# Kernel tuning notes

Hardware: AMD Instinct MI355X
Metric: run time of the kernel (lower is better)

The kernel has to match this reference:

```python
import jax, jax.numpy as jnp
import numpy as np

B, T, C, H = 8, 1024, 768, 12
HD = C // H
EPS = 1e-5
NEG = jnp.finfo(jnp.float32).min


def layer_norm(x, scale, bias):
    mu = jnp.mean(x, axis=-1, keepdims=True)
    var = jnp.mean(jnp.square(x - mu), axis=-1, keepdims=True)
    return (x - mu) * jax.lax.rsqrt(var + EPS) * scale + bias


def setup_inputs() -> dict:
    key = jax.random.key(0)
    ks = jax.random.split(key, 8)
    s = lambda fan_in: 1.0 / np.sqrt(fan_in)
    x = jax.random.normal(ks[0], (B, T, C), dtype=jnp.float32)
    mask = jnp.tril(jnp.ones((T, T), dtype=bool))[None, None, :, :]
    return {
        "x": x,
        "mask": mask,
        "ln1_scale": jnp.ones((C,), jnp.float32),
        "ln1_bias": jnp.zeros((C,), jnp.float32),
        "w_qkv": jax.random.normal(ks[1], (C, 3 * C), jnp.float32) * s(C),
        "b_qkv": jnp.zeros((3 * C,), jnp.float32),
        "w_attn_proj": jax.random.normal(ks[2], (C, C), jnp.float32) * s(C),
        "b_attn_proj": jnp.zeros((C,), jnp.float32),
        "ln2_scale": jnp.ones((C,), jnp.float32),
        "ln2_bias": jnp.zeros((C,), jnp.float32),
        "w_fc": jax.random.normal(ks[3], (C, 4 * C), jnp.float32) * s(C),
        "b_fc": jnp.zeros((4 * C,), jnp.float32),
        "w_mlp_proj": jax.random.normal(ks[4], (4 * C, C), jnp.float32) * s(4 * C),
        "b_mlp_proj": jnp.zeros((C,), jnp.float32),
    }


def reference(x, mask, ln1_scale, ln1_bias, w_qkv, b_qkv, w_attn_proj,
              b_attn_proj, ln2_scale, ln2_bias, w_fc, b_fc, w_mlp_proj,
              b_mlp_proj):
    # --- attention branch (pre-LN) ---
    h = layer_norm(x, ln1_scale, ln1_bias)
    qkv = jnp.einsum('btc,cd->btd', h, w_qkv) + b_qkv      # [B,T,3C]
    qkv = qkv.reshape(B, T, 3 * H, HD)
    q, k, v = jnp.array_split(qkv, 3, axis=2)              # each [B,T,H,HD]
    scale = 1.0 / jnp.sqrt(jnp.float32(HD))
    attn = jnp.einsum('bqhd,bkhd->bhqk', q, k) * scale     # [B,H,T,T]
    attn = jnp.where(mask, attn, NEG)
    attn = jax.nn.softmax(attn, axis=-1)
    ctx = jnp.einsum('bhqk,bkhd->bqhd', attn, v).reshape(B, T, C)
    attn_out = jnp.einsum('btc,cd->btd', ctx, w_attn_proj) + b_attn_proj
    x = x + attn_out
    # --- MLP branch (pre-LN) ---
    h = layer_norm(x, ln2_scale, ln2_bias)
    h = jax.nn.gelu(jnp.einsum('btc,cf->btf', h, w_fc) + b_fc)  # tanh approx, as flax default
    mlp_out = jnp.einsum('btf,fc->btc', h, w_mlp_proj) + b_mlp_proj
    return x + mlp_out
```

## Files before the change

kernel.cpp:

```cpp
#include <hip/hip_runtime.h>
#include <hip/hip_bf16.h>
#include <cstdint>
#include <math.h>

#define BB 8
#define TT 1024
#define CC 768
#define HH 12
#define MROWS (BB*TT)

typedef __hip_bfloat16 bf16;
typedef __attribute__((ext_vector_type(8))) __bf16 bf16x8;
typedef __attribute__((ext_vector_type(4))) float f32x4;

#define MFMA16(a,b,c) __builtin_amdgcn_mfma_f32_16x16x32_bf16(a,b,c,0,0,0)

__device__ __forceinline__ void lds_barrier() {
  asm volatile("s_waitcnt lgkmcnt(0)\n\ts_barrier" ::: "memory");
}

__global__ __launch_bounds__(256) void ln_kernel(
    const float* __restrict__ x, const float* __restrict__ scale,
    const float* __restrict__ bias, bf16* __restrict__ out)
{
  int row = blockIdx.x;
  const float* xr = x + (size_t)row * CC;
  float v[3];
  float s = 0.f, s2 = 0.f;
  for (int i = 0; i < 3; i++) {
    v[i] = xr[threadIdx.x + i*256];
    s += v[i]; s2 += v[i]*v[i];
  }
  for (int m = 1; m < 64; m <<= 1) { s += __shfl_xor(s, m); s2 += __shfl_xor(s2, m); }
  __shared__ float ssum[4], ssum2[4];
  int w = threadIdx.x >> 6;
  if ((threadIdx.x & 63) == 0) { ssum[w] = s; ssum2[w] = s2; }
  __syncthreads();
  s = ssum[0]+ssum[1]+ssum[2]+ssum[3];
  s2 = ssum2[0]+ssum2[1]+ssum2[2]+ssum2[3];
  float mu = s * (1.f/CC);
  float var = s2 * (1.f/CC) - mu*mu;
  float rs = rsqrtf(var + 1e-5f);
  bf16* orow = out + (size_t)row * CC;
  for (int i = 0; i < 3; i++) {
    int c = threadIdx.x + i*256;
    orow[c] = __float2bfloat16((v[i]-mu)*rs*scale[c] + bias[c]);
  }
}

__global__ __launch_bounds__(256) void wtrans_all(
    const float* __restrict__ s0, const float* __restrict__ s1,
    const float* __restrict__ s2, const float* __restrict__ s3,
    bf16* __restrict__ d0, bf16* __restrict__ d1,
    bf16* __restrict__ d2, bf16* __restrict__ d3)
{
  int bid = blockIdx.x;
  const float* src; bf16* dst; int K, N, r;
  if (bid < 1728)      { src = s0; dst = d0; K = 768;  N = 2304; r = bid; }
  else if (bid < 2304) { src = s1; dst = d1; K = 768;  N = 768;  r = bid - 1728; }
  else if (bid < 4608) { src = s2; dst = d2; K = 768;  N = 3072; r = bid - 2304; }
  else                 { src = s3; dst = d3; K = 3072; N = 768;  r = bid - 4608; }
  int nbx = N >> 5;
  int bx = r % nbx, by = r / nbx;
  __shared__ float tile[32][33];
  int n0 = bx * 32, k0 = by * 32;
  int tx = threadIdx.x & 31, ty = threadIdx.x >> 5;
  for (int i = 0; i < 4; i++)
    tile[ty + i*8][tx] = src[(size_t)(k0 + ty + i*8)*N + n0 + tx];
  __syncthreads();
  for (int i = 0; i < 4; i++)
    dst[(size_t)(n0 + ty + i*8)*K + k0 + tx] = __float2bfloat16(tile[tx][ty + i*8]);
}

__global__ __launch_bounds__(256) void vtrans_kernel(
    const bf16* __restrict__ src, bf16* __restrict__ dst)
{
  __shared__ bf16 tile[64][65];
  int bh = blockIdx.x >> 4, t0 = (blockIdx.x & 15) * 64;
  const bf16* s = src + ((size_t)bh * TT + t0) * 64;
  for (int i = 0; i < 16; i++) {
    int idx = threadIdx.x + i*256;
    tile[idx >> 6][idx & 63] = s[idx];
  }
  __syncthreads();
  bf16* o = dst + (size_t)bh * 64 * TT + t0;
  for (int i = 0; i < 16; i++) {
    int idx = threadIdx.x + i*256;
    int d = idx >> 6, t = idx & 63;
    o[(size_t)d * TT + t] = tile[t][d];
  }
}

template<int EPI>
__global__ __launch_bounds__(256) void gemm_bt(
    const bf16* __restrict__ A, const bf16* __restrict__ Bt,
    const float* __restrict__ bias, int Mdim, int Ndim, int Kdim,
    const float* __restrict__ res, void* __restrict__ out0,
    bf16* __restrict__ outK, bf16* __restrict__ outV)
{
  __shared__ bf16 As[2][128*32];
  __shared__ bf16 Bs[2][128*32];
  int tid = threadIdx.x;
  int wave = tid >> 6, lane = tid & 63;
  int quad = lane >> 4, l15 = lane & 15;
  int wr = wave >> 1, wc = wave & 1;

  int Nb = gridDim.x;
  int lin = blockIdx.y * Nb + blockIdx.x;
  int band = lin / (8*Nb);
  int rem  = lin - band*8*Nb;
  int m0 = (band*8 + (rem & 7)) * 128;
  int n0 = (rem >> 3) * 128;

  const int sub = lane >> 2;
  const int kk = (lane & 3) * 8;

  f32x4 acc[4][4];
  for (int i = 0; i < 4; i++) for (int j = 0; j < 4; j++)
    acc[i][j] = (f32x4){0.f,0.f,0.f,0.f};

  const bf16* pa0 = A  + (size_t)(m0 + wave*16      + sub)*Kdim + kk;
  const bf16* pa1 = A  + (size_t)(m0 + (4+wave)*16  + sub)*Kdim + kk;
  const bf16* pb0 = Bt + (size_t)(n0 + wave*16      + sub)*Kdim + kk;
  const bf16* pb1 = Bt + (size_t)(n0 + (4+wave)*16  + sub)*Kdim + kk;
  const int wslot = (lane & 3) ^ ((lane >> 3) & 3);
  const int woff0 = wave*512     + sub*32 + wslot*8;
  const int woff1 = (4+wave)*512 + sub*32 + wslot*8;

  const int rsw = (quad ^ ((l15 >> 1) & 3)) * 8;

  const int niter = Kdim >> 5;
  const int nd = niter >> 1;

#define LOADSET(ra0_,ra1_,rb0_,rb1_) do { \
    ra0_ = *reinterpret_cast<const bf16x8*>(pa0); \
    ra1_ = *reinterpret_cast<const bf16x8*>(pa1); \
    rb0_ = *reinterpret_cast<const bf16x8*>(pb0); \
    rb1_ = *reinterpret_cast<const bf16x8*>(pb1); \
    pa0 += 32; pa1 += 32; pb0 += 32; pb1 += 32; } while(0)

#define WRITESET(buf,ra0_,ra1_,rb0_,rb1_) do { \
    *reinterpret_cast<bf16x8*>(As[buf] + woff0) = ra0_; \
    *reinterpret_cast<bf16x8*>(As[buf] + woff1) = ra1_; \
    *reinterpret_cast<bf16x8*>(Bs[buf] + woff0) = rb0_; \
    *reinterpret_cast<bf16x8*>(Bs[buf] + woff1) = rb1_; } while(0)

#define COMPUTE(buf) do { \
    bf16x8 bfr[4]; \
    for (int j = 0; j < 4; j++) \
      bfr[j] = *reinterpret_cast<const bf16x8*>(Bs[buf] + (wc*64 + j*16 + l15)*32 + rsw); \
    for (int i = 0; i < 4; i++) { \
      bf16x8 af = *reinterpret_cast<const bf16x8*>(As[buf] + (wr*64 + i*16 + l15)*32 + rsw); \
      for (int j = 0; j < 4; j++) \
        acc[i][j] = MFMA16(af, bfr[j], acc[i][j]); \
    } } while(0)

  bf16x8 rAa0, rAa1, rAb0, rAb1;
  bf16x8 rBa0, rBa1, rBb0, rBb1;
  LOADSET(rAa0, rAa1, rAb0, rAb1);
  LOADSET(rBa0, rBa1, rBb0, rBb1);
  WRITESET(0, rAa0, rAa1, rAb0, rAb1);
  lds_barrier();

  for (int d = 0; d < nd; d++) {
    bool mA = (2*d + 2 < niter);
    bool mB = (2*d + 3 < niter);
    if (mA) LOADSET(rAa0, rAa1, rAb0, rAb1);
    COMPUTE(0);
    WRITESET(1, rBa0, rBa1, rBb0, rBb1);
    lds_barrier();
    if (mB) LOADSET(rBa0, rBa1, rBb0, rBb1);
    COMPUTE(1);
    if (mA) {
      WRITESET(0, rAa0, rAa1, rAb0, rAb1);
      lds_barrier();
    }
  }
#undef LOADSET
#undef WRITESET
#undef COMPUTE

  for (int i = 0; i < 4; i++) {
    for (int j = 0; j < 4; j++) {
      for (int r = 0; r < 4; r++) {
        int row = m0 + wr*64 + i*16 + quad*4 + r;
        int col = n0 + wc*64 + j*16 + l15;
        float cv = acc[i][j][r] + bias[col];
        if (EPI == 0) {
          int part = col / 768;
          int cc = col - part*768;
          int h = cc >> 6, d = cc & 63;
          int b = row >> 10, t = row & 1023;
          bf16* dst = (part == 0) ? (bf16*)out0 : (part == 1) ? outK : outV;
          dst[(((size_t)(b*HH + h))*TT + t)*64 + d] = __float2bfloat16(cv);
        } else if (EPI == 1) {
          ((float*)out0)[(size_t)row*Ndim + col] = cv + res[(size_t)row*Ndim + col];
        } else {
          float u = cv;
          float y = 0.7978845608f*(u + 0.044715f*u*u*u);
          float e = __expf(2.f*fabsf(y));
          float z = 2.f/(e + 1.f);
          float sel = (y >= 0.f) ? (2.f - z) : z;
          ((bf16*)out0)[(size_t)row*Ndim + col] = __float2bfloat16(0.5f*u*sel);
        }
      }
    }
  }
}

__global__ __launch_bounds__(512) void attn_kernel(
    const bf16* __restrict__ Q, const bf16* __restrict__ Kb,
    const bf16* __restrict__ Vt, bf16* __restrict__ ctx)
{
  __shared__ bf16 Ks[64*64];
  __shared__ bf16 Vs[64*64];
  __shared__ bf16 Ps[8*16*64];

  int tid = threadIdx.x, wave = tid >> 6, lane = tid & 63;
  int quad = lane >> 4, l15 = lane & 15;
  int bh = blockIdx.x >> 3;
  int tile = 7 - (blockIdx.x & 7);
  int q0b = tile*128;
  int q0w = q0b + wave*16;
  int b = bh / HH, h = bh - b*HH;
  const bf16* Qp = Q + ((size_t)bh*TT + q0w)*64;
  const bf16* Kp = Kb + (size_t)bh*TT*64;
  const bf16* Vp = Vt + (size_t)bh*64*TT;
  bf16* Pw = Ps + wave*16*64;

  bf16x8 qf[2];
  qf[0] = *reinterpret_cast<const bf16x8*>(Qp + l15*64 + quad*8);
  qf[1] = *reinterpret_cast<const bf16x8*>(Qp + l15*64 + 32 + quad*8);

  f32x4 O[4];
  for (int j = 0; j < 4; j++) O[j] = (f32x4){0.f,0.f,0.f,0.f};
  float lsum[4] = {0.f, 0.f, 0.f, 0.f};
  const float c2 = 0.18033688f;

  const int srow = tid >> 3;
  const int sc   = tid & 7;
  const int ph   = sc ^ (srow & 7);

  int nc = 2*tile + 2;

  bf16x8 kreg, vreg, kreg2, vreg2;
  kreg = *reinterpret_cast<const bf16x8*>(Kp + (size_t)srow*64 + sc*8);
  vreg = *reinterpret_cast<const bf16x8*>(Vp + (size_t)srow*TT + sc*8);

  for (int ci = 0; ci < nc; ci++) {
    int kbase = ci*64;
    __syncthreads();
    *reinterpret_cast<bf16x8*>(Ks + srow*64 + ph*8) = kreg;
    *reinterpret_cast<bf16x8*>(Vs + srow*64 + ph*8) = vreg;
    if (ci + 1 < nc) {
      int kb2 = kbase + 64;
      kreg2 = *reinterpret_cast<const bf16x8*>(Kp + (size_t)(kb2 + srow)*64 + sc*8);
      vreg2 = *reinterpret_cast<const bf16x8*>(Vp + (size_t)srow*TT + kb2 + sc*8);
    }
    __syncthreads();

    f32x4 S[4];
    for (int j = 0; j < 4; j++) S[j] = (f32x4){0.f,0.f,0.f,0.f};
    for (int kh = 0; kh < 2; kh++) {
      for (int j = 0; j < 4; j++) {
        int key = j*16 + l15;
        bf16x8 kf = *reinterpret_cast<const bf16x8*>(
            Ks + key*64 + ((kh*4 + quad) ^ (key & 7))*8);
        S[j] = MFMA16(qf[kh], kf, S[j]);
      }
    }

    float p[4][4];
    if (kbase + 63 > q0w) {
      for (int j = 0; j < 4; j++) {
        int key = kbase + j*16 + l15;
        for (int r = 0; r < 4; r++) {
          int row = q0w + quad*4 + r;
          p[j][r] = (key <= row) ? __builtin_amdgcn_exp2f(S[j][r]*c2) : 0.f;
        }
      }
    } else {
      for (int j = 0; j < 4; j++)
        for (int r = 0; r < 4; r++)
          p[j][r] = __builtin_amdgcn_exp2f(S[j][r]*c2);
    }
    for (int j = 0; j < 4; j++)
      for (int r = 0; r < 4; r++) lsum[r] += p[j][r];

    for (int j = 0; j < 4; j++) {
      int cblk = j*2 + (l15 >> 3);
      int koff = l15 & 7;
      for (int r = 0; r < 4; r++) {
        int q = quad*4 + r;
        Pw[q*64 + (cblk ^ (q & 7))*8 + koff] = __float2bfloat16(p[j][r]);
      }
    }

    for (int kh = 0; kh < 2; kh++) {
      bf16x8 pf = *reinterpret_cast<const bf16x8*>(
          Pw + l15*64 + ((kh*4 + quad) ^ (l15 & 7))*8);
      for (int j = 0; j < 4; j++) {
        int d = j*16 + l15;
        bf16x8 vf = *reinterpret_cast<const bf16x8*>(
            Vs + d*64 + ((kh*4 + quad) ^ (d & 7))*8);
        O[j] = MFMA16(pf, vf, O[j]);
      }
    }

    kreg = kreg2; vreg = vreg2;
  }

  for (int r = 0; r < 4; r++)
    for (int msk = 1; msk < 16; msk <<= 1)
      lsum[r] += __shfl_xor(lsum[r], msk);

  bf16* cp = ctx + ((size_t)b*TT + q0w)*CC + h*64;
  for (int r = 0; r < 4; r++) {
    float inv = 1.f / lsum[r];
    int row = quad*4 + r;
    for (int j = 0; j < 4; j++)
      cp[(size_t)row*CC + j*16 + l15] = __float2bfloat16(O[j][r]*inv);
  }
}

extern "C" void kernel_launch(void* const* d_in, const int* in_sizes, int n_in,
                              void* d_out, int out_size, void* d_ws, size_t ws_size,
                              hipStream_t stream)
{
  const float* x    = (const float*)d_in[0];
  const float* ln1s = (const float*)d_in[2];
  const float* ln1b = (const float*)d_in[3];
  const float* wqkv = (const float*)d_in[4];
  const float* bqkv = (const float*)d_in[5];
  const float* wap  = (const float*)d_in[6];
  const float* bap  = (const float*)d_in[7];
  const float* ln2s = (const float*)d_in[8];
  const float* ln2b = (const float*)d_in[9];
  const float* wfc  = (const float*)d_in[10];
  const float* bfc  = (const float*)d_in[11];
  const float* wmp  = (const float*)d_in[12];
  const float* bmp  = (const float*)d_in[13];

  char* ws = (char*)d_ws;
  bf16* wqkv_t = (bf16*)ws; ws += (size_t)2304*768*2;
  bf16* wap_t  = (bf16*)ws; ws += (size_t)768*768*2;
  bf16* wfc_t  = (bf16*)ws; ws += (size_t)3072*768*2;
  bf16* wmp_t  = (bf16*)ws; ws += (size_t)768*3072*2;
  bf16* buf1   = (bf16*)ws; ws += (size_t)MROWS*CC*2;
  bf16* Qb     = (bf16*)ws; ws += (size_t)MROWS*CC*2;
  bf16* Kbuf   = (bf16*)ws; ws += (size_t)MROWS*CC*2;
  bf16* Vb     = (bf16*)ws; ws += (size_t)MROWS*CC*2;
  bf16* Vt     = (bf16*)ws; ws += (size_t)MROWS*CC*2;
  bf16* g      = Qb;
  float* r1    = (float*)ws; ws += (size_t)MROWS*CC*4;

  dim3 blk(256);
  wtrans_all<<<6912, blk, 0, stream>>>(wqkv, wap, wfc, wmp,
                                       wqkv_t, wap_t, wfc_t, wmp_t);
  ln_kernel<<<MROWS, blk, 0, stream>>>(x, ln1s, ln1b, buf1);
  gemm_bt<0><<<dim3(2304/128, MROWS/128), blk, 0, stream>>>(
      buf1, wqkv_t, bqkv, MROWS, 2304, 768, nullptr, (void*)Qb, Kbuf, Vb);
  vtrans_kernel<<<BB*HH*16, blk, 0, stream>>>(Vb, Vt);
  attn_kernel<<<BB*HH*8, dim3(512), 0, stream>>>(Qb, Kbuf, Vt, buf1);
  gemm_bt<1><<<dim3(768/128, MROWS/128), blk, 0, stream>>>(
      buf1, wap_t, bap, MROWS, 768, 768, x, (void*)r1, nullptr, nullptr);
  ln_kernel<<<MROWS, blk, 0, stream>>>(r1, ln2s, ln2b, buf1);
  gemm_bt<2><<<dim3(3072/128, MROWS/128), blk, 0, stream>>>(
      buf1, wfc_t, bfc, MROWS, 3072, 768, nullptr, (void*)g, nullptr, nullptr);
  gemm_bt<1><<<dim3(768/128, MROWS/128), blk, 0, stream>>>(
      g, wmp_t, bmp, MROWS, 768, 3072, r1, d_out, nullptr, nullptr);
}
```

Measured before the change: 356.4 us.

## Widen GEMM K-tile to 64 with single-stage register prefetch and XOR swizzle

Doubles the K depth of each shared-memory tile in the bf16 GEMM from 32 to 64. The two-register-set double pipeline is replaced by one prefetch set of eight vector loads per step, and the LDS swizzle changes to an 8-way XOR. This halves the number of barriers and loop iterations per K and gives more MFMA work between syncs. In exchange LDS use doubles to 64KB per block, which may lower occupancy, and register pressure rises.

```diff
diff --git a/kernel.cpp b/kernel.cpp
--- a/kernel.cpp
+++ b/kernel.cpp
@@ -98,8 +98,8 @@
     const float* __restrict__ res, void* __restrict__ out0,
     bf16* __restrict__ outK, bf16* __restrict__ outV)
 {
-  __shared__ bf16 As[2][128*32];
-  __shared__ bf16 Bs[2][128*32];
+  __shared__ bf16 As[2][128*64];
+  __shared__ bf16 Bs[2][128*64];
   int tid = threadIdx.x;
   int wave = tid >> 6, lane = tid & 63;
   int quad = lane >> 4, l15 = lane & 15;
@@ -112,67 +112,76 @@
   int m0 = (band*8 + (rem & 7)) * 128;
   int n0 = (rem >> 3) * 128;
 
-  const int sub = lane >> 2;
-  const int kk = (lane & 3) * 8;
+  const int srow = lane >> 2;
+  const int scol = (lane & 3) * 8;
 
   f32x4 acc[4][4];
   for (int i = 0; i < 4; i++) for (int j = 0; j < 4; j++)
     acc[i][j] = (f32x4){0.f,0.f,0.f,0.f};
 
-  const bf16* pa0 = A  + (size_t)(m0 + wave*16      + sub)*Kdim + kk;
-  const bf16* pa1 = A  + (size_t)(m0 + (4+wave)*16  + sub)*Kdim + kk;
-  const bf16* pb0 = Bt + (size_t)(n0 + wave*16      + sub)*Kdim + kk;
-  const bf16* pb1 = Bt + (size_t)(n0 + (4+wave)*16  + sub)*Kdim + kk;
-  const int wslot = (lane & 3) ^ ((lane >> 3) & 3);
-  const int woff0 = wave*512     + sub*32 + wslot*8;
-  const int woff1 = (4+wave)*512 + sub*32 + wslot*8;
-
-  const int rsw = (quad ^ ((l15 >> 1) & 3)) * 8;
-
-  const int niter = Kdim >> 5;
-  const int nd = niter >> 1;
-
-#define LOADSET(ra0_,ra1_,rb0_,rb1_) do { \
-    ra0_ = *reinterpret_cast<const bf16x8*>(pa0); \
-    ra1_ = *reinterpret_cast<const bf16x8*>(pa1); \
-    rb0_ = *reinterpret_cast<const bf16x8*>(pb0); \
-    rb1_ = *reinterpret_cast<const bf16x8*>(pb1); \
-    pa0 += 32; pa1 += 32; pb0 += 32; pb1 += 32; } while(0)
-
-#define WRITESET(buf,ra0_,ra1_,rb0_,rb1_) do { \
-    *reinterpret_cast<bf16x8*>(As[buf] + woff0) = ra0_; \
-    *reinterpret_cast<bf16x8*>(As[buf] + woff1) = ra1_; \
-    *reinterpret_cast<bf16x8*>(Bs[buf] + woff0) = rb0_; \
-    *reinterpret_cast<bf16x8*>(Bs[buf] + woff1) = rb1_; } while(0)
+  const bf16* pa0 = A  + (size_t)(m0 + wave*16      + srow)*Kdim + scol;
+  const bf16* pa1 = A  + (size_t)(m0 + 64 + wave*16 + srow)*Kdim + scol;
+  const bf16* pb0 = Bt + (size_t)(n0 + wave*16      + srow)*Kdim + scol;
+  const bf16* pb1 = Bt + (size_t)(n0 + 64 + wave*16 + srow)*Kdim + scol;
+
+  const int xr = srow & 7;
+  const int woff = (wave*16 + srow)*64 + ((lane & 3) ^ xr)*8;
+
+  const int rsw = (quad ^ (l15 & 7)) * 8;
+
+  const int niter = Kdim >> 6;
+
+  bf16x8 ra0, ra1, ra2, ra3, rb0, rb1, rb2, rb3;
+
+#define LOADSET() do { \
+    ra0 = *reinterpret_cast<const bf16x8*>(pa0); \
+    ra1 = *reinterpret_cast<const bf16x8*>(pa0 + 32); \
+    ra2 = *reinterpret_cast<const bf16x8*>(pa1); \
+    ra3 = *reinterpret_cast<const bf16x8*>(pa1 + 32); \
+    rb0 = *reinterpret_cast<const bf16x8*>(pb0); \
+    rb1 = *reinterpret_cast<const bf16x8*>(pb0 + 32); \
+    rb2 = *reinterpret_cast<const bf16x8*>(pb1); \
+    rb3 = *reinterpret_cast<const bf16x8*>(pb1 + 32); \
+    pa0 += 64; pa1 += 64; pb0 += 64; pb1 += 64; } while(0)
+
+#define WRITESET(buf) do { \
+    *reinterpret_cast<bf16x8*>(As[buf] + woff)          = ra0; \
+    *reinterpret_cast<bf16x8*>(As[buf] + (woff ^ 32))   = ra1; \
+    *reinterpret_cast<bf16x8*>(As[buf] + 4096 + woff)        = ra2; \
+    *reinterpret_cast<bf16x8*>(As[buf] + 4096 + (woff ^ 32)) = ra3; \
+    *reinterpret_cast<bf16x8*>(Bs[buf] + woff)          = rb0; \
+    *reinterpret_cast<bf16x8*>(Bs[buf] + (woff ^ 32))   = rb1; \
+    *reinterpret_cast<bf16x8*>(Bs[buf] + 4096 + woff)        = rb2; \
+    *reinterpret_cast<bf16x8*>(Bs[buf] + 4096 + (woff ^ 32)) = rb3; } while(0)
 
 #define COMPUTE(buf) do { \
-    bf16x8 bfr[4]; \
-    for (int j = 0; j < 4; j++) \
-      bfr[j] = *reinterpret_cast<const bf16x8*>(Bs[buf] + (wc*64 + j*16 + l15)*32 + rsw); \
-    for (int i = 0; i < 4; i++) { \
-      bf16x8 af = *reinterpret_cast<const bf16x8*>(As[buf] + (wr*64 + i*16 + l15)*32 + rsw); \
+    _Pragma("unroll") \
+    for (int kh = 0; kh < 2; kh++) { \
+      const int ks = kh * 32; \
+      bf16x8 bfr[4]; \
+      _Pragma("unroll") \
       for (int j = 0; j < 4; j++) \
-        acc[i][j] = MFMA16(af, bfr[j], acc[i][j]); \
+        bfr[j] = *reinterpret_cast<const bf16x8*>(Bs[buf] + (wc*64 + j*16 + l15)*64 + (rsw ^ ks)); \
+      _Pragma("unroll") \
+      for (int i = 0; i < 4; i++) { \
+        bf16x8 af = *reinterpret_cast<const bf16x8*>(As[buf] + (wr*64 + i*16 + l15)*64 + (rsw ^ ks)); \
+        _Pragma("unroll") \
+        for (int j = 0; j < 4; j++) \
+          acc[i][j] = MFMA16(af, bfr[j], acc[i][j]); \
+      } \
     } } while(0)
 
-  bf16x8 rAa0, rAa1, rAb0, rAb1;
-  bf16x8 rBa0, rBa1, rBb0, rBb1;
-  LOADSET(rAa0, rAa1, rAb0, rAb1);
-  LOADSET(rBa0, rBa1, rBb0, rBb1);
-  WRITESET(0, rAa0, rAa1, rAb0, rAb1);
+  LOADSET();
+  WRITESET(0);
   lds_barrier();
 
-  for (int d = 0; d < nd; d++) {
-    bool mA = (2*d + 2 < niter);
-    bool mB = (2*d + 3 < niter);
-    if (mA) LOADSET(rAa0, rAa1, rAb0, rAb1);
-    COMPUTE(0);
-    WRITESET(1, rBa0, rBa1, rBb0, rBb1);
-    lds_barrier();
-    if (mB) LOADSET(rBa0, rBa1, rBb0, rBb1);
-    COMPUTE(1);
-    if (mA) {
-      WRITESET(0, rAa0, rAa1, rAb0, rAb1);
+  for (int it = 0; it < niter; it++) {
+    int cur = it & 1, nxt = cur ^ 1;
+    bool more = (it + 1 < niter);
+    if (more) LOADSET();
+    COMPUTE(cur);
+    if (more) {
+      WRITESET(nxt);
       lds_barrier();
     }
   }
```

After: 365.3 us. +2.5%, slower.
